# Optimization experiments

Measured on AMD Instinct MI355X. Metric: run time of the kernel, lower is better.

## Reference

```python
import jax, jax.numpy as jnp
import numpy as np

B, N, D, M, L = 64, 4096, 128, 1024, 128  # batch, set size, d_in, num_ref_points, num_projections


def setup_inputs() -> dict:
    key = jax.random.key(0)
    k1, k2, k3, k4 = jax.random.split(key, 4)
    X = jax.random.normal(k1, (B, N, D), dtype=jnp.float32)
    theta_v = jax.random.normal(k2, (L, D), dtype=jnp.float32)          # weight_norm 'v' param
    ref_points = jax.random.normal(k3, (M, L), dtype=jnp.float32)       # self.reference
    weight = jax.random.normal(k4, (L, M), dtype=jnp.float32) * 0.04    # xavier-ish self.weight
    return {"X": X, "theta_v": theta_v, "ref_points": ref_points, "weight": weight}


def reference(X, theta_v, ref_points, weight):
    # weight_norm(dim=0) with g fixed to 1: effective row-normalized projection matrix
    W = theta_v / jnp.linalg.norm(theta_v, axis=1, keepdims=True)       # [L, D]
    slices = jnp.einsum('bnd,ld->bnl', X, W)                            # [B, N, L]
    s = jnp.sort(slices, axis=1)                                        # sort each slice over the set dim

    # M != N: linear interp of sorted values onto the M-point grid (torchinterp1d equivalent;
    # xnew range is strictly inside x range since M < N, so clamping never triggers)
    x = jnp.linspace(0.0, 1.0, N + 2)[1:-1]                             # [N]
    xnew = jnp.linspace(0.0, 1.0, M + 2)[1:-1]                          # [M]
    y = jnp.transpose(s, (0, 2, 1)).reshape(B * L, N)                   # [B*L, N]
    interp = jax.vmap(lambda yr: jnp.interp(xnew, x, yr))(y)            # [B*L, M]
    interp = jnp.transpose(interp.reshape(B, L, M), (0, 2, 1))          # [B, M, L]

    # gather interpolated quantiles by the sort order of the reference set
    Rind = jnp.argsort(ref_points, axis=0)                              # [M, L]
    gathered = jnp.take_along_axis(interp, jnp.broadcast_to(Rind[None], (B, M, L)), axis=1)
    diff = ref_points[None, :, :] - gathered                            # [B, M, L]

    # weighted sum over reference points per projection
    return jnp.einsum('bml,lm->bl', diff, weight)                       # [B, L]
```

## Files before the change

### kernel.cpp

```cpp
#include <hip/hip_runtime.h>

static constexpr int Bc = 64;
static constexpr int Nc = 4096;
static constexpr int Dc = 128;
static constexpr int Mc = 1024;
static constexpr int Lc = 128;

using short8   = __attribute__((ext_vector_type(8))) short;
using ushort8v = __attribute__((ext_vector_type(8))) unsigned short;
using f32x4    = __attribute__((ext_vector_type(4))) float;

__device__ __forceinline__ unsigned short f2bf(float x) {
  unsigned u = __builtin_bit_cast(unsigned, x);
  return (unsigned short)((u + 0x7FFFu + ((u >> 16) & 1u)) >> 16);
}
__device__ __forceinline__ float bf2f(unsigned short h) {
  unsigned u = ((unsigned)h) << 16;
  return __builtin_bit_cast(float, u);
}

__device__ __forceinline__ int swz(int i) { return i ^ ((i >> 4) & 31); }

__global__ __launch_bounds__(256) void setup_kernel(
    const float* __restrict__ theta_v, const float* __restrict__ ref,
    const float* __restrict__ weight, unsigned short* __restrict__ Wh,
    unsigned short* __restrict__ Wl, float* __restrict__ C,
    float* __restrict__ v) {
  constexpr int NBv = 2048;
  constexpr float LOv = -4.2f;
  constexpr float SCv = (float)NBv / 8.4f;

  __shared__ int pref[NBv];
  __shared__ float skey[Mc];
  __shared__ unsigned short sidx[Mc];
  __shared__ float vrow[Nc];
  __shared__ int wsum[4];
  __shared__ float s2[2];
  __shared__ float c4[4];

  int l = blockIdx.x;
  int tid = threadIdx.x;
  int lane = tid & 63, wv = tid >> 6;

  float x[4];
  #pragma unroll
  for (int j = 0; j < 4; ++j) x[j] = ref[(size_t)(tid + 256 * j) * Lc + l];

  for (int i = tid; i < NBv; i += 256) pref[i] = 0;
  for (int i = tid; i < Nc; i += 256) vrow[i] = 0.f;

  float wval = 0.f;
  if (tid < Dc) {
    wval = theta_v[l * Dc + tid];
    float sq = wval * wval;
    #pragma unroll
    for (int off = 1; off < 64; off <<= 1) sq += __shfl_xor(sq, off, 64);
    if (lane == 0) s2[wv] = sq;
  }
  {
    float cacc = 0.f;
    #pragma unroll
    for (int j = 0; j < 4; ++j) cacc += x[j] * weight[(size_t)l * Mc + tid + 256 * j];
    #pragma unroll
    for (int off = 1; off < 64; off <<= 1) cacc += __shfl_xor(cacc, off, 64);
    if (lane == 0) c4[wv] = cacc;
  }
  __syncthreads();

  if (tid < Dc) {
    float norm = sqrtf(s2[0] + s2[1]);
    float val = wval / norm;
    unsigned short hi = f2bf(val);
    Wh[l * Dc + tid] = hi;
    Wl[l * Dc + tid] = f2bf(val - bf2f(hi));
  }
  if (tid == 0) C[l] = c4[0] + c4[1] + c4[2] + c4[3];

  int bb[4];
  #pragma unroll
  for (int j = 0; j < 4; ++j) {
    int bi = (int)((x[j] - LOv) * SCv);
    bi = bi < 0 ? 0 : (bi > NBv - 1 ? NBv - 1 : bi);
    bb[j] = bi;
    atomicAdd(&pref[swz(bi)], 1);
  }
  __syncthreads();

  {
    int base_ = tid * 8;
    int loc[8]; int s = 0;
    #pragma unroll
    for (int j = 0; j < 8; ++j) loc[j] = pref[swz(base_ + j)];
    #pragma unroll
    for (int j = 0; j < 8; ++j) { int c = loc[j]; loc[j] = s; s += c; }
    int inc = s;
    #pragma unroll
    for (int off = 1; off < 64; off <<= 1) {
      int o = __shfl_up(inc, off, 64);
      if (lane >= off) inc += o;
    }
    if (lane == 63) wsum[wv] = inc;
    __syncthreads();
    int wbase = 0;
    #pragma unroll
    for (int ww = 0; ww < 4; ++ww) if (ww < wv) wbase += wsum[ww];
    int tbase = wbase + inc - s;
    #pragma unroll
    for (int j = 0; j < 8; ++j) pref[swz(base_ + j)] = tbase + loc[j];
  }
  __syncthreads();

  #pragma unroll
  for (int j = 0; j < 4; ++j) {
    int p = atomicAdd(&pref[swz(bb[j])], 1);
    skey[p] = x[j];
    sidx[p] = (unsigned short)(tid + 256 * j);
  }
  __syncthreads();

  #pragma unroll
  for (int k = 0; k < 4; ++k) {
    int p = tid + 256 * k;
    float y = skey[p];
    int m = sidx[p];
    int b = (int)((y - LOv) * SCv);
    b = b < 0 ? 0 : (b > NBv - 1 ? NBv - 1 : b);
    int lo_ = b ? pref[swz(b - 1)] : 0;
    int hi_ = pref[swz(b)];
    int r = lo_;
    for (int q = lo_; q < hi_; ++q) {
      float z = skey[q];
      r += (z < y || (z == y && sidx[q] < m)) ? 1 : 0;
    }
    float wvv = weight[(size_t)l * Mc + r];
    double pos = (double)(m + 1) * (double)(Nc + 1) / (double)(Mc + 1) - 1.0;
    int i0 = (int)pos;
    float t = (float)(pos - (double)i0);
    atomicAdd(&vrow[i0], (1.0f - t) * wvv);
    atomicAdd(&vrow[i0 + 1], t * wvv);
  }
  __syncthreads();
  for (int i = tid; i < Nc; i += 256) v[(size_t)l * Nc + i] = vrow[i];
}

__global__ __launch_bounds__(256) void gemm_kernel(
    const float* __restrict__ X, const unsigned short* __restrict__ Whp,
    const unsigned short* __restrict__ Wlp, float* __restrict__ sl) {
  __shared__ unsigned short Bh[128][40];
  __shared__ unsigned short Bl[128][40];

  int bloc = blockIdx.y;
  int nbase = blockIdx.x * 128;
  int tid = threadIdx.x;
  int lane = tid & 63;
  int w = tid >> 6;
  int m16 = lane & 15;
  int kg = lane >> 4;

  const float* arow0 = X + ((size_t)bloc * Nc + nbase + w * 32 + m16) * Dc;
  const float* arow1 = arow0 + (size_t)16 * Dc;

  f32x4 acc[2][8] = {};

  for (int d0 = 0; d0 < Dc; d0 += 32) {
    __syncthreads();
    #pragma unroll
    for (int s = 0; s < 2; ++s) {
      int idx = tid * 2 + s;
      int row = idx >> 2;
      int c = (idx & 3) * 8;
      *(ushort8v*)&Bh[row][c] = *(const ushort8v*)(Whp + (size_t)row * Dc + d0 + c);
      *(ushort8v*)&Bl[row][c] = *(const ushort8v*)(Wlp + (size_t)row * Dc + d0 + c);
    }
    __syncthreads();

    short8 ah[2], al[2];
    #pragma unroll
    for (int t = 0; t < 2; ++t) {
      const float* ap = (t ? arow1 : arow0) + d0 + kg * 8;
      float4 f0 = *(const float4*)ap;
      float4 f1 = *(const float4*)(ap + 4);
      float xs[8] = {f0.x, f0.y, f0.z, f0.w, f1.x, f1.y, f1.z, f1.w};
      short8 hi, lo;
      #pragma unroll
      for (int e = 0; e < 8; ++e) {
        unsigned short h = f2bf(xs[e]);
        hi[e] = (short)h;
        lo[e] = (short)f2bf(xs[e] - bf2f(h));
      }
      ah[t] = hi; al[t] = lo;
    }

    #pragma unroll
    for (int u = 0; u < 8; ++u) {
      short8 bh = *(const short8*)&Bh[u * 16 + m16][kg * 8];
      short8 bl = *(const short8*)&Bl[u * 16 + m16][kg * 8];
      #pragma unroll
      for (int t = 0; t < 2; ++t) {
        acc[t][u] = __builtin_amdgcn_mfma_f32_16x16x32_bf16(ah[t], bh, acc[t][u], 0, 0, 0);
        acc[t][u] = __builtin_amdgcn_mfma_f32_16x16x32_bf16(ah[t], bl, acc[t][u], 0, 0, 0);
        acc[t][u] = __builtin_amdgcn_mfma_f32_16x16x32_bf16(al[t], bh, acc[t][u], 0, 0, 0);
      }
    }
  }

  #pragma unroll
  for (int t = 0; t < 2; ++t) {
    #pragma unroll
    for (int u = 0; u < 8; ++u) {
      int l = u * 16 + m16;
      int n0 = nbase + w * 32 + t * 16 + kg * 4;
      float* dst = sl + ((size_t)bloc * Lc + l) * Nc + n0;
      *(float4*)dst = *(float4*)&acc[t][u];
    }
  }
}

__global__ __launch_bounds__(512, 8) void rank_dot_kernel(
    const float* __restrict__ sl, const float* __restrict__ v,
    const float* __restrict__ C, float* __restrict__ out, int b0) {
  constexpr int NB = 4096;
  constexpr float LO = -4.2f;
  constexpr float SCALE = (float)NB / 8.4f;
  constexpr int NT = 512;
  constexpr int EL = Nc / NT;

  __shared__ int pref[NB];
  __shared__ float skey[Nc];
  int* wsum = (int*)skey;
  float* red = (float*)pref;

  int l = blockIdx.x & (Lc - 1);
  int bloc = blockIdx.x >> 7;
  int tid = threadIdx.x;
  const float* src = sl + ((size_t)bloc * Lc + l) * Nc;

  float x[EL];
  {
    const float4* s4 = (const float4*)src;
    #pragma unroll
    for (int j = 0; j < EL / 4; ++j) {
      float4 f = s4[tid + NT * j];
      x[j * 4 + 0] = f.x; x[j * 4 + 1] = f.y;
      x[j * 4 + 2] = f.z; x[j * 4 + 3] = f.w;
    }
  }

  for (int i = tid; i < NB; i += NT) pref[i] = 0;
  __syncthreads();

  int bb[EL];
  #pragma unroll
  for (int j = 0; j < EL; ++j) {
    int bi = (int)((x[j] - LO) * SCALE);
    bi = bi < 0 ? 0 : (bi > NB - 1 ? NB - 1 : bi);
    bb[j] = bi;
    atomicAdd(&pref[swz(bi)], 1);
  }
  __syncthreads();

  {
    int base_ = tid * 8;
    int loc[8]; int s = 0;
    #pragma unroll
    for (int j = 0; j < 8; ++j) loc[j] = pref[swz(base_ + j)];
    #pragma unroll
    for (int j = 0; j < 8; ++j) { int c = loc[j]; loc[j] = s; s += c; }
    int lane = tid & 63, wv = tid >> 6;
    int inc = s;
    #pragma unroll
    for (int off = 1; off < 64; off <<= 1) {
      int o = __shfl_up(inc, off, 64);
      if (lane >= off) inc += o;
    }
    if (lane == 63) wsum[wv] = inc;
    __syncthreads();
    int wbase = 0;
    #pragma unroll
    for (int ww = 0; ww < 8; ++ww) if (ww < wv) wbase += wsum[ww];
    int tbase = wbase + inc - s;
    #pragma unroll
    for (int j = 0; j < 8; ++j) pref[swz(base_ + j)] = tbase + loc[j];
  }
  __syncthreads();

  #pragma unroll
  for (int j = 0; j < EL; ++j) {
    int p = atomicAdd(&pref[swz(bb[j])], 1);
    skey[p] = x[j];
  }
  __syncthreads();

  const float* vrow = v + (size_t)l * Nc;
  float acc = 0.f;
  #pragma unroll
  for (int k = 0; k < EL; ++k) {
    int p = tid + NT * k;
    float y = skey[p];
    int b = (int)((y - LO) * SCALE);
    b = b < 0 ? 0 : (b > NB - 1 ? NB - 1 : b);
    int lo_ = b ? pref[swz(b - 1)] : 0;
    int hi_ = pref[swz(b)];
    int r = lo_;
    for (int q = lo_; q < hi_; ++q) {
      float z = skey[q];
      r += (z < y || (z == y && q < p)) ? 1 : 0;
    }
    acc += y * vrow[r];
  }

  #pragma unroll
  for (int off = 1; off < 64; off <<= 1) acc += __shfl_xor(acc, off, 64);
  __syncthreads();
  if ((tid & 63) == 0) red[tid >> 6] = acc;
  __syncthreads();
  if (tid == 0) {
    float t = 0.f;
    #pragma unroll
    for (int ww = 0; ww < 8; ++ww) t += red[ww];
    int b = b0 + bloc;
    out[(size_t)b * Lc + l] = C[l] - t;
  }
}

extern "C" void kernel_launch(void* const* d_in, const int* in_sizes, int n_in,
                              void* d_out, int out_size, void* d_ws, size_t ws_size,
                              hipStream_t stream) {
  const float* X       = (const float*)d_in[0];
  const float* theta_v = (const float*)d_in[1];
  const float* ref     = (const float*)d_in[2];
  const float* weight  = (const float*)d_in[3];
  float* out = (float*)d_out;

  float* v  = (float*)d_ws;
  unsigned short* Wh = (unsigned short*)(v + (size_t)Lc * Nc);
  unsigned short* Wl = Wh + (size_t)Lc * Dc;
  float* Cc = (float*)(Wl + (size_t)Lc * Dc);
  float* sl = Cc + 128;
  size_t used = (size_t)((char*)sl - (char*)d_ws);
  size_t per_b = (size_t)Lc * Nc * sizeof(float);
  int chunk = 1;
  if (ws_size > used + per_b) {
    size_t c = (ws_size - used) / per_b;
    chunk = (int)(c > (size_t)Bc ? (size_t)Bc : c);
    if (chunk < 1) chunk = 1;
  }

  setup_kernel<<<Lc, 256, 0, stream>>>(theta_v, ref, weight, Wh, Wl, Cc, v);

  for (int b0 = 0; b0 < Bc; b0 += chunk) {
    int nb = (Bc - b0) < chunk ? (Bc - b0) : chunk;
    dim3 g1(Nc / 128, nb);
    gemm_kernel<<<g1, 256, 0, stream>>>(X + (size_t)b0 * Nc * Dc, Wh, Wl, sl);
    rank_dot_kernel<<<(size_t)nb * Lc, 512, 0, stream>>>(sl, v, Cc, out, b0);
  }
}
```

Measured before the change: 174.0 us.

## Double-buffer GEMM B tiles, use 512 threads, and reuse scatter offsets in rank kernel

The GEMM kernel moves to 512 threads with one 16-row tile per wave. It prefetches all of its X row data into registers up front and double-buffers the W hi/lo tiles in shared memory, so the next tile loads while MFMAs run, with one barrier per k-step. In the rank kernel, the histogram atomic's return value is kept as a per-element offset, so the scatter needs no second atomic. The rank pass then works on each thread's own elements, using bucket bounds taken from the exclusive prefix. The cost is more registers and twice the LDS, and the ordering of ties within a bucket now follows atomic order instead of sorted index.

```diff
diff --git a/kernel.cpp b/kernel.cpp
--- a/kernel.cpp
+++ b/kernel.cpp
@@ -143,76 +143,81 @@
   for (int i = tid; i < Nc; i += 256) v[(size_t)l * Nc + i] = vrow[i];
 }
 
-__global__ __launch_bounds__(256) void gemm_kernel(
+__global__ __launch_bounds__(512) void gemm_kernel(
     const float* __restrict__ X, const unsigned short* __restrict__ Whp,
     const unsigned short* __restrict__ Wlp, float* __restrict__ sl) {
-  __shared__ unsigned short Bh[128][40];
-  __shared__ unsigned short Bl[128][40];
+  __shared__ unsigned short Bh[2][128][40];
+  __shared__ unsigned short Bl[2][128][40];
 
   int bloc = blockIdx.y;
   int nbase = blockIdx.x * 128;
   int tid = threadIdx.x;
   int lane = tid & 63;
-  int w = tid >> 6;
+  int wv = tid >> 6;
   int m16 = lane & 15;
   int kg = lane >> 4;
 
-  const float* arow0 = X + ((size_t)bloc * Nc + nbase + w * 32 + m16) * Dc;
-  const float* arow1 = arow0 + (size_t)16 * Dc;
-
-  f32x4 acc[2][8] = {};
-
-  for (int d0 = 0; d0 < Dc; d0 += 32) {
+  int brow = tid >> 2;
+  int bc = (tid & 3) * 8;
+  const unsigned short* gbh = Whp + (size_t)brow * Dc + bc;
+  const unsigned short* gbl = Wlp + (size_t)brow * Dc + bc;
+
+  const float* arow = X + ((size_t)bloc * Nc + nbase + wv * 16 + m16) * Dc + kg * 8;
+  float4 af[4][2];
+  #pragma unroll
+  for (int c = 0; c < 4; ++c) {
+    af[c][0] = *(const float4*)(arow + c * 32);
+    af[c][1] = *(const float4*)(arow + c * 32 + 4);
+  }
+
+  ushort8v rbh = *(const ushort8v*)gbh;
+  ushort8v rbl = *(const ushort8v*)gbl;
+  *(ushort8v*)&Bh[0][brow][bc] = rbh;
+  *(ushort8v*)&Bl[0][brow][bc] = rbl;
+  rbh = *(const ushort8v*)(gbh + 32);
+  rbl = *(const ushort8v*)(gbl + 32);
+
+  f32x4 acc[8] = {};
+  __syncthreads();
+
+  #pragma unroll
+  for (int c = 0; c < 4; ++c) {
+    if (c < 3) {
+      *(ushort8v*)&Bh[(c + 1) & 1][brow][bc] = rbh;
+      *(ushort8v*)&Bl[(c + 1) & 1][brow][bc] = rbl;
+    }
+    if (c < 2) {
+      rbh = *(const ushort8v*)(gbh + (c + 2) * 32);
+      rbl = *(const ushort8v*)(gbl + (c + 2) * 32);
+    }
+
+    float xs[8] = {af[c][0].x, af[c][0].y, af[c][0].z, af[c][0].w,
+                   af[c][1].x, af[c][1].y, af[c][1].z, af[c][1].w};
+    short8 ah, al;
+    #pragma unroll
+    for (int e = 0; e < 8; ++e) {
+      unsigned short h = f2bf(xs[e]);
+      ah[e] = (short)h;
+      al[e] = (short)f2bf(xs[e] - bf2f(h));
+    }
+
+    #pragma unroll
+    for (int u = 0; u < 8; ++u) {
+      short8 bh = *(const short8*)&Bh[c & 1][u * 16 + m16][kg * 8];
+      short8 bl = *(const short8*)&Bl[c & 1][u * 16 + m16][kg * 8];
+      acc[u] = __builtin_amdgcn_mfma_f32_16x16x32_bf16(ah, bh, acc[u], 0, 0, 0);
+      acc[u] = __builtin_amdgcn_mfma_f32_16x16x32_bf16(ah, bl, acc[u], 0, 0, 0);
+      acc[u] = __builtin_amdgcn_mfma_f32_16x16x32_bf16(al, bh, acc[u], 0, 0, 0);
+    }
     __syncthreads();
-    #pragma unroll
-    for (int s = 0; s < 2; ++s) {
-      int idx = tid * 2 + s;
-      int row = idx >> 2;
-      int c = (idx & 3) * 8;
-      *(ushort8v*)&Bh[row][c] = *(const ushort8v*)(Whp + (size_t)row * Dc + d0 + c);
-      *(ushort8v*)&Bl[row][c] = *(const ushort8v*)(Wlp + (size_t)row * Dc + d0 + c);
-    }
-    __syncthreads();
-
-    short8 ah[2], al[2];
-    #pragma unroll
-    for (int t = 0; t < 2; ++t) {
-      const float* ap = (t ? arow1 : arow0) + d0 + kg * 8;
-      float4 f0 = *(const float4*)ap;
-      float4 f1 = *(const float4*)(ap + 4);
-      float xs[8] = {f0.x, f0.y, f0.z, f0.w, f1.x, f1.y, f1.z, f1.w};
-      short8 hi, lo;
-      #pragma unroll
-      for (int e = 0; e < 8; ++e) {
-        unsigned short h = f2bf(xs[e]);
-        hi[e] = (short)h;
-        lo[e] = (short)f2bf(xs[e] - bf2f(h));
-      }
-      ah[t] = hi; al[t] = lo;
-    }
-
-    #pragma unroll
-    for (int u = 0; u < 8; ++u) {
-      short8 bh = *(const short8*)&Bh[u * 16 + m16][kg * 8];
-      short8 bl = *(const short8*)&Bl[u * 16 + m16][kg * 8];
-      #pragma unroll
-      for (int t = 0; t < 2; ++t) {
-        acc[t][u] = __builtin_amdgcn_mfma_f32_16x16x32_bf16(ah[t], bh, acc[t][u], 0, 0, 0);
-        acc[t][u] = __builtin_amdgcn_mfma_f32_16x16x32_bf16(ah[t], bl, acc[t][u], 0, 0, 0);
-        acc[t][u] = __builtin_amdgcn_mfma_f32_16x16x32_bf16(al[t], bh, acc[t][u], 0, 0, 0);
-      }
-    }
-  }
-
-  #pragma unroll
-  for (int t = 0; t < 2; ++t) {
-    #pragma unroll
-    for (int u = 0; u < 8; ++u) {
-      int l = u * 16 + m16;
-      int n0 = nbase + w * 32 + t * 16 + kg * 4;
-      float* dst = sl + ((size_t)bloc * Lc + l) * Nc + n0;
-      *(float4*)dst = *(float4*)&acc[t][u];
-    }
+  }
+
+  #pragma unroll
+  for (int u = 0; u < 8; ++u) {
+    int l = u * 16 + m16;
+    int n0 = nbase + wv * 16 + kg * 4;
+    float* dst = sl + ((size_t)bloc * Lc + l) * Nc + n0;
+    *(float4*)dst = *(float4*)&acc[u];
   }
 }
 
@@ -250,12 +255,13 @@
   __syncthreads();
 
   int bb[EL];
+  int ofs[EL];
   #pragma unroll
   for (int j = 0; j < EL; ++j) {
     int bi = (int)((x[j] - LO) * SCALE);
     bi = bi < 0 ? 0 : (bi > NB - 1 ? NB - 1 : bi);
     bb[j] = bi;
-    atomicAdd(&pref[swz(bi)], 1);
+    ofs[j] = atomicAdd(&pref[swz(bi)], 1);
   }
   __syncthreads();
 
@@ -266,41 +272,41 @@
     for (int j = 0; j < 8; ++j) loc[j] = pref[swz(base_ + j)];
     #pragma unroll
     for (int j = 0; j < 8; ++j) { int c = loc[j]; loc[j] = s; s += c; }
-    int lane = tid & 63, wv = tid >> 6;
+    int lane = tid & 63, wvv = tid >> 6;
     int inc = s;
     #pragma unroll
     for (int off = 1; off < 64; off <<= 1) {
       int o = __shfl_up(inc, off, 64);
       if (lane >= off) inc += o;
     }
-    if (lane == 63) wsum[wv] = inc;
+    if (lane == 63) wsum[wvv] = inc;
     __syncthreads();
     int wbase = 0;
     #pragma unroll
-    for (int ww = 0; ww < 8; ++ww) if (ww < wv) wbase += wsum[ww];
+    for (int ww = 0; ww < 8; ++ww) if (ww < wvv) wbase += wsum[ww];
     int tbase = wbase + inc - s;
     #pragma unroll
     for (int j = 0; j < 8; ++j) pref[swz(base_ + j)] = tbase + loc[j];
   }
   __syncthreads();
 
+  int pos[EL];
   #pragma unroll
   for (int j = 0; j < EL; ++j) {
-    int p = atomicAdd(&pref[swz(bb[j])], 1);
-    skey[p] = x[j];
+    pos[j] = pref[swz(bb[j])] + ofs[j];
+    skey[pos[j]] = x[j];
   }
   __syncthreads();
 
   const float* vrow = v + (size_t)l * Nc;
   float acc = 0.f;
   #pragma unroll
-  for (int k = 0; k < EL; ++k) {
-    int p = tid + NT * k;
-    float y = skey[p];
-    int b = (int)((y - LO) * SCALE);
-    b = b < 0 ? 0 : (b > NB - 1 ? NB - 1 : b);
-    int lo_ = b ? pref[swz(b - 1)] : 0;
-    int hi_ = pref[swz(b)];
+  for (int j = 0; j < EL; ++j) {
+    float y = x[j];
+    int b = bb[j];
+    int p = pos[j];
+    int lo_ = pref[swz(b)];
+    int hi_ = (b == NB - 1) ? Nc : pref[swz(b + 1)];
     int r = lo_;
     for (int q = lo_; q < hi_; ++q) {
       float z = skey[q];
@@ -351,7 +357,7 @@
   for (int b0 = 0; b0 < Bc; b0 += chunk) {
     int nb = (Bc - b0) < chunk ? (Bc - b0) : chunk;
     dim3 g1(Nc / 128, nb);
-    gemm_kernel<<<g1, 256, 0, stream>>>(X + (size_t)b0 * Nc * Dc, Wh, Wl, sl);
+    gemm_kernel<<<g1, 512, 0, stream>>>(X + (size_t)b0 * Nc * Dc, Wh, Wl, sl);
     rank_dot_kernel<<<(size_t)nb * Lc, 512, 0, stream>>>(sl, v, Cc, out, b0);
   }
 }
```

Result: slower. 192.0 us (+10.4%).
